# Kernel tuning notes

Measured on AMD Instinct MI355X. Metric: run time of the kernel, lower is better.

The kernel has to match this reference:

```python
import jax, jax.numpy as jnp
import numpy as np

B, S, D_MODEL = 4, 1024, 1024
HEADS, D_KEY, D_VAL = 16, 64, 64


def setup_inputs() -> dict:
    key = jax.random.key(0)
    ks = jax.random.split(key, 8)
    # glorot-ish scaled params
    sk = 1.0 / np.sqrt(D_MODEL)
    X = jax.random.normal(ks[0], (B, S, D_MODEL), dtype=jnp.float32)
    Wk = jax.random.normal(ks[1], (HEADS, D_MODEL, D_KEY), dtype=jnp.float32) * sk
    Wq = jax.random.normal(ks[2], (HEADS, D_MODEL, D_KEY), dtype=jnp.float32) * sk
    Wv = jax.random.normal(ks[3], (HEADS, D_MODEL, D_VAL), dtype=jnp.float32) * sk
    bk = jnp.zeros((HEADS, D_KEY), dtype=jnp.float32)
    bq = jnp.zeros((HEADS, D_KEY), dtype=jnp.float32)
    bv = jnp.zeros((HEADS, D_VAL), dtype=jnp.float32)
    Wo = jax.random.normal(ks[4], (HEADS * D_VAL, D_MODEL), dtype=jnp.float32) * (1.0 / np.sqrt(HEADS * D_VAL))
    bo = jnp.zeros((D_MODEL,), dtype=jnp.float32)
    return {"X": X, "Wk": Wk, "bk": bk, "Wq": Wq, "bq": bq, "Wv": Wv, "bv": bv, "Wo": Wo, "bo": bo}


def reference(X, Wk, bk, Wq, bq, Wv, bv, Wo, bo):
    # Per-head projections, batched over heads (original loops in Python)
    K = jnp.einsum('bsd,hdk->bhsk', X, Wk) + bk[None, :, None, :]
    Q = jnp.einsum('bsd,hdk->bhsk', X, Wq) + bq[None, :, None, :]
    V = jnp.einsum('bsd,hdv->bhsv', X, Wv) + bv[None, :, None, :]
    d_k = K.shape[-1]
    scores = jnp.einsum('bhqk,bhsk->bhqs', Q, K) / jnp.sqrt(jnp.asarray(d_k, X.dtype))
    A = jax.nn.softmax(scores, axis=-1)           # [B,H,S,S]
    Z = jnp.einsum('bhqs,bhsv->bhqv', A, V)        # [B,H,S,Dv]
    # concat heads: [B,S,H*Dv]
    Zc = jnp.transpose(Z, (0, 2, 1, 3)).reshape(X.shape[0], X.shape[1], -1)
    # output projection + residual; dropout is identity at inference
    return Zc @ Wo + bo + X
```

## Files before the change

### kernel.cpp

```cpp
#include <hip/hip_runtime.h>
#include <hip/hip_bf16.h>

typedef __bf16 bf16x8 __attribute__((ext_vector_type(8)));
typedef float f32x4 __attribute__((ext_vector_type(4)));
typedef unsigned short u16;
typedef u16 u16x4 __attribute__((ext_vector_type(4)));
typedef u16 u16x8 __attribute__((ext_vector_type(8)));

#define LDA 72

__device__ inline u16 f2bf(float f) {
    union { float f; unsigned u; } v; v.f = f;
    unsigned r = v.u + 0x7fffu + ((v.u >> 16) & 1u);
    return (u16)(r >> 16);
}

#define GLD16(g, l) __builtin_amdgcn_global_load_lds( \
    (const __attribute__((address_space(1))) unsigned int*)(g), \
    (__attribute__((address_space(3))) unsigned int*)(l), 16, 0, 0)

__global__ void k_prep(const float* __restrict__ X, u16* __restrict__ Xb,
                       const float* __restrict__ Wk, const float* __restrict__ Wq,
                       const float* __restrict__ Wv, u16* __restrict__ WT,
                       const float* __restrict__ Wo, u16* __restrict__ WoT) {
    __shared__ u16 Ls[64 * LDA];
    int u = blockIdx.x, tid = threadIdx.x;
    if (u < 4096) {
        int idx = u * 256 + tid;
        float4 v = *(const float4*)&X[(size_t)idx * 4];
        u16x4 o; o.x = f2bf(v.x); o.y = f2bf(v.y); o.z = f2bf(v.z); o.w = f2bf(v.w);
        *(u16x4*)&Xb[(size_t)idx * 4] = o;
    } else if (u < 4864) {
        int b2 = u - 4096;
        int dt = b2 & 15, h = (b2 >> 4) & 15, p = b2 >> 8;
        const float* src = (p == 0 ? Wk : p == 1 ? Wq : Wv);
        int r0 = tid >> 4, c4 = tid & 15;
        for (int j = 0; j < 4; j++) {
            int d = r0 + j * 16;
            float4 v = *(const float4*)&src[((size_t)h * 1024 + dt * 64 + d) * 64 + c4 * 4];
            u16* q = &Ls[d * LDA + c4 * 4];
            q[0] = f2bf(v.x); q[1] = f2bf(v.y); q[2] = f2bf(v.z); q[3] = f2bf(v.w);
        }
        __syncthreads();
        int nk = tid >> 2, cd = tid & 3;
        u16 tmp[16];
        for (int j = 0; j < 16; j++) tmp[j] = Ls[(cd * 16 + j) * LDA + nk];
        size_t o = ((size_t)(p * 1024 + h * 64 + nk)) * 1024 + dt * 64 + cd * 16;
        *(u16x8*)&WT[o] = *(u16x8*)&tmp[0];
        *(u16x8*)&WT[o + 8] = *(u16x8*)&tmp[8];
    } else {
        int b2 = u - 4864;
        int dt = b2 & 15, nt2 = b2 >> 4;
        int r0 = tid >> 4, c4 = tid & 15;
        for (int j = 0; j < 4; j++) {
            int d = r0 + j * 16;
            float4 v = *(const float4*)&Wo[(size_t)(dt * 64 + d) * 1024 + nt2 * 64 + c4 * 4];
            u16* q = &Ls[d * LDA + c4 * 4];
            q[0] = f2bf(v.x); q[1] = f2bf(v.y); q[2] = f2bf(v.z); q[3] = f2bf(v.w);
        }
        __syncthreads();
        int nr = tid >> 2, cd = tid & 3;
        u16 tmp[16];
        for (int j = 0; j < 16; j++) tmp[j] = Ls[(cd * 16 + j) * LDA + nr];
        size_t o = ((size_t)(nt2 * 64 + nr)) * 1024 + dt * 64 + cd * 16;
        *(u16x8*)&WoT[o] = *(u16x8*)&tmp[0];
        *(u16x8*)&WoT[o + 8] = *(u16x8*)&tmp[8];
    }
}

__global__ __launch_bounds__(256, 3) void k_qkv(
    const u16* __restrict__ Xb, const u16* __restrict__ WT,
    const float* __restrict__ bk, const float* __restrict__ bq, const float* __restrict__ bv,
    u16* __restrict__ Kw, u16* __restrict__ Qw, u16* __restrict__ Vtw)
{
    __shared__ u16 As[128 * 64];
    __shared__ u16 Bs[128 * 64];
    int tid = threadIdx.x, w = tid >> 6, lane = tid & 63, quad = lane >> 4, l16 = lane & 15;
    int wm = w & 1, wn = w >> 1;
    int m0 = blockIdx.x * 128, n0 = blockIdx.y * 128;
    int rl = lane >> 3, ch = lane & 7, swch = ch ^ rl;
    const u16* Ag = Xb + (size_t)(m0 + w * 32 + rl) * 1024 + swch * 8;
    const u16* Bg = WT + (size_t)(n0 + w * 32 + rl) * 1024 + swch * 8;

    int hb = blockIdx.y * 2 + wn;
    int p = hb >> 4, hh = hb & 15;
    bool ct = (p < 2);

    f32x4 acc[4][4] = {};
    for (int k0 = 0; k0 < 1024; k0 += 64) {
        for (int i = 0; i < 4; i++) {
            GLD16(Ag + (size_t)i * 8 * 1024 + k0, &As[(w * 32 + i * 8) * 64]);
            GLD16(Bg + (size_t)i * 8 * 1024 + k0, &Bs[(w * 32 + i * 8) * 64]);
        }
        __syncthreads();
        for (int ks = 0; ks < 2; ks++) {
            bf16x8 af[4], bf[4];
            int c = (ks << 2) | quad;
            for (int mt = 0; mt < 4; mt++) {
                int row = wm * 64 + mt * 16 + l16;
                af[mt] = *(bf16x8*)&As[row * 64 + (c ^ (row & 7)) * 8];
            }
            for (int nt = 0; nt < 4; nt++) {
                int row = wn * 64 + nt * 16 + l16;
                bf[nt] = *(bf16x8*)&Bs[row * 64 + (c ^ (row & 7)) * 8];
            }
            if (ct) {
                for (int mt = 0; mt < 4; mt++)
                    for (int nt = 0; nt < 4; nt++)
                        acc[mt][nt] = __builtin_amdgcn_mfma_f32_16x16x32_bf16(bf[nt], af[mt], acc[mt][nt], 0, 0, 0);
            } else {
                for (int mt = 0; mt < 4; mt++)
                    for (int nt = 0; nt < 4; nt++)
                        acc[mt][nt] = __builtin_amdgcn_mfma_f32_16x16x32_bf16(af[mt], bf[nt], acc[mt][nt], 0, 0, 0);
            }
        }
        __syncthreads();
    }
    const float* bias = (p == 0 ? bk : p == 1 ? bq : bv) + hh * 64;
    if (ct) {
        u16* dst = (p == 0) ? Kw : Qw;
        float sc = (p == 0) ? 0.125f : 1.0f;
        for (int mt = 0; mt < 4; mt++) {
            int m = m0 + wm * 64 + mt * 16 + l16;
            int b = m >> 10, s = m & 1023;
            size_t base = ((size_t)((b << 4) + hh) * 1024 + s) * 64;
            for (int nt = 0; nt < 4; nt++) {
                float4 bb = *(const float4*)&bias[nt * 16 + quad * 4];
                u16x4 o;
                o[0] = f2bf((acc[mt][nt][0] + bb.x) * sc);
                o[1] = f2bf((acc[mt][nt][1] + bb.y) * sc);
                o[2] = f2bf((acc[mt][nt][2] + bb.z) * sc);
                o[3] = f2bf((acc[mt][nt][3] + bb.w) * sc);
                *(u16x4*)&dst[base + nt * 16 + quad * 4] = o;
            }
        }
    } else {
        for (int mt = 0; mt < 4; mt++)
            for (int nt = 0; nt < 4; nt++) {
                int nk = nt * 16 + l16;
                float bb = bias[nk];
                int mb = m0 + wm * 64 + mt * 16 + quad * 4;
                int b = mb >> 10, s = mb & 1023;
                u16x4 o;
                for (int r = 0; r < 4; r++) o[r] = f2bf(acc[mt][nt][r] + bb);
                *(u16x4*)&Vtw[((size_t)((b << 4) + hh) * 64 + nk) * 1024 + s] = o;
            }
    }
}

__global__ __launch_bounds__(256) void k_attn(
    const u16* __restrict__ Qw, const u16* __restrict__ Kw,
    const u16* __restrict__ Vtw, u16* __restrict__ Zw)
{
    __shared__ u16 Ks[2][64 * 64];
    __shared__ u16 Vs[2][64 * 64];
    __shared__ u16 Ps[4 * 2 * 16 * LDA];
    int tid = threadIdx.x, w = tid >> 6, lane = tid & 63, quad = lane >> 4, l16 = lane & 15;
    int bh = blockIdx.x, q0 = blockIdx.y * 128;
    const u16* Qp = Qw + (size_t)bh * 65536;
    int rl = lane >> 3, ch = lane & 7, swch = ch ^ rl;
    const u16* Kg = Kw + (size_t)bh * 65536 + (w * 16 + rl) * 64 + swch * 8;
    const u16* Vg = Vtw + (size_t)bh * 65536 + (size_t)(w * 16 + rl) * 1024 + swch * 8;

    bf16x8 aq[2][2];
    for (int g = 0; g < 2; g++)
        for (int ks = 0; ks < 2; ks++)
            aq[g][ks] = *(const bf16x8*)&Qp[(size_t)(q0 + w * 32 + g * 16 + l16) * 64 + ks * 32 + quad * 8];

    f32x4 acc[2][4] = {};
    f32x4 accs[2] = {};
    __bf16 onev = (__bf16)1.0f;
    bf16x8 ones = {onev, onev, onev, onev, onev, onev, onev, onev};
    u16* Pw0 = Ps + (w * 2) * 16 * LDA;
    u16* Pw1 = Pw0 + 16 * LDA;

#define STAGE(st, buf) { int s0_ = (st) * 64; \
    for (int i = 0; i < 2; i++) { \
        GLD16(Kg + (s0_ + i * 8) * 64, &Ks[buf][(w * 16 + i * 8) * 64]); \
        GLD16(Vg + (size_t)i * 8 * 1024 + s0_, &Vs[buf][(w * 16 + i * 8) * 64]); } }

    STAGE(0, 0);
    for (int st = 0; st < 16; st++) {
        int buf = st & 1;
        __syncthreads();
        if (st < 15) STAGE(st + 1, buf ^ 1);
        f32x4 sacc[2][4] = {};
        for (int ks = 0; ks < 2; ks++) {
            int c = (ks << 2) | quad;
            for (int nt = 0; nt < 4; nt++) {
                int row = nt * 16 + l16;
                bf16x8 kf = *(bf16x8*)&Ks[buf][row * 64 + (c ^ (row & 7)) * 8];
                sacc[0][nt] = __builtin_amdgcn_mfma_f32_16x16x32_bf16(aq[0][ks], kf, sacc[0][nt], 0, 0, 0);
                sacc[1][nt] = __builtin_amdgcn_mfma_f32_16x16x32_bf16(aq[1][ks], kf, sacc[1][nt], 0, 0, 0);
            }
        }
        for (int g = 0; g < 2; g++) {
            u16* Pw = g ? Pw1 : Pw0;
            for (int nt = 0; nt < 4; nt++)
                for (int r = 0; r < 4; r++) {
                    float p = __builtin_exp2f(__builtin_fmaf(sacc[g][nt][r], 1.44269504f, -23.0831206f));
                    union { float f; unsigned u; } cv; cv.f = p;
                    Pw[(quad * 4 + r) * LDA + nt * 16 + l16] = (u16)((cv.u + 0x8000u) >> 16);
                }
        }
        for (int ks2 = 0; ks2 < 2; ks2++) {
            int c = (ks2 << 2) | quad;
            bf16x8 ap0 = *(bf16x8*)&Pw0[l16 * LDA + ks2 * 32 + quad * 8];
            bf16x8 ap1 = *(bf16x8*)&Pw1[l16 * LDA + ks2 * 32 + quad * 8];
            accs[0] = __builtin_amdgcn_mfma_f32_16x16x32_bf16(ap0, ones, accs[0], 0, 0, 0);
            accs[1] = __builtin_amdgcn_mfma_f32_16x16x32_bf16(ap1, ones, accs[1], 0, 0, 0);
            for (int ntv = 0; ntv < 4; ntv++) {
                int row = ntv * 16 + l16;
                bf16x8 vf = *(bf16x8*)&Vs[buf][row * 64 + (c ^ (row & 7)) * 8];
                acc[0][ntv] = __builtin_amdgcn_mfma_f32_16x16x32_bf16(ap0, vf, acc[0][ntv], 0, 0, 0);
                acc[1][ntv] = __builtin_amdgcn_mfma_f32_16x16x32_bf16(ap1, vf, acc[1][ntv], 0, 0, 0);
            }
        }
    }
#undef STAGE
    int b = bh >> 4, h = bh & 15;
    for (int g = 0; g < 2; g++)
        for (int r = 0; r < 4; r++) {
            float inv = 1.f / accs[g][r];
            int q = q0 + w * 32 + g * 16 + quad * 4 + r;
            for (int ntv = 0; ntv < 4; ntv++)
                Zw[((size_t)(b * 1024 + q)) * 1024 + h * 64 + ntv * 16 + l16] = f2bf(acc[g][ntv][r] * inv);
        }
}

__global__ __launch_bounds__(256) void k_oproj(
    const u16* __restrict__ Zw, const u16* __restrict__ WoT, const float* __restrict__ bo,
    const float* __restrict__ X, float* __restrict__ out)
{
    __shared__ u16 As[64 * 64];
    __shared__ u16 Bs[128 * 64];
    int tid = threadIdx.x, w = tid >> 6, lane = tid & 63, quad = lane >> 4, l16 = lane & 15;
    int wm = w & 1, wn = w >> 1;
    int m0 = blockIdx.x * 64, n0 = blockIdx.y * 128;
    int rl = lane >> 3, ch = lane & 7, swch = ch ^ rl;
    const u16* Ag = Zw + (size_t)(m0 + w * 16 + rl) * 1024 + swch * 8;
    const u16* Bg = WoT + (size_t)(n0 + w * 32 + rl) * 1024 + swch * 8;

    f32x4 acc[2][4] = {};
    for (int k0 = 0; k0 < 1024; k0 += 64) {
        for (int i = 0; i < 2; i++)
            GLD16(Ag + (size_t)i * 8 * 1024 + k0, &As[(w * 16 + i * 8) * 64]);
        for (int i = 0; i < 4; i++)
            GLD16(Bg + (size_t)i * 8 * 1024 + k0, &Bs[(w * 32 + i * 8) * 64]);
        __syncthreads();
        for (int ks = 0; ks < 2; ks++) {
            bf16x8 af[2], bf[4];
            int c = (ks << 2) | quad;
            for (int mt = 0; mt < 2; mt++) {
                int row = wm * 32 + mt * 16 + l16;
                af[mt] = *(bf16x8*)&As[row * 64 + (c ^ (row & 7)) * 8];
            }
            for (int nt = 0; nt < 4; nt++) {
                int row = wn * 64 + nt * 16 + l16;
                bf[nt] = *(bf16x8*)&Bs[row * 64 + (c ^ (row & 7)) * 8];
            }
            for (int mt = 0; mt < 2; mt++)
                for (int nt = 0; nt < 4; nt++)
                    acc[mt][nt] = __builtin_amdgcn_mfma_f32_16x16x32_bf16(af[mt], bf[nt], acc[mt][nt], 0, 0, 0);
        }
        __syncthreads();
    }
    for (int mt = 0; mt < 2; mt++)
        for (int nt = 0; nt < 4; nt++) {
            int n = n0 + wn * 64 + nt * 16 + l16;
            float bb = bo[n];
            for (int r = 0; r < 4; r++) {
                int m = m0 + wm * 32 + mt * 16 + quad * 4 + r;
                out[(size_t)m * 1024 + n] = acc[mt][nt][r] + bb + X[(size_t)m * 1024 + n];
            }
        }
}

extern "C" void kernel_launch(void* const* d_in, const int* in_sizes, int n_in,
                              void* d_out, int out_size, void* d_ws, size_t ws_size,
                              hipStream_t stream) {
    const float* X  = (const float*)d_in[0];
    const float* Wk = (const float*)d_in[1];
    const float* bk = (const float*)d_in[2];
    const float* Wq = (const float*)d_in[3];
    const float* bq = (const float*)d_in[4];
    const float* Wv = (const float*)d_in[5];
    const float* bv = (const float*)d_in[6];
    const float* Wo = (const float*)d_in[7];
    const float* bo = (const float*)d_in[8];
    u16* ws = (u16*)d_ws;
    const size_t NQ = 4u * 16u * 1024u * 64u;
    u16* Qw  = ws;
    u16* Kw  = ws + NQ;
    u16* Vtw = ws + 2 * NQ;
    u16* Zw  = ws + 3 * NQ;
    u16* WT  = ws + 4 * NQ;
    u16* WoT = WT + 3 * 1048576;
    u16* Xb  = WoT + 1048576;
    float* outp = (float*)d_out;

    k_prep <<<5120, 256, 0, stream>>>(X, Xb, Wk, Wq, Wv, WT, Wo, WoT);
    k_qkv  <<<dim3(32, 24), 256, 0, stream>>>(Xb, WT, bk, bq, bv, Kw, Qw, Vtw);
    k_attn <<<dim3(64, 8), 256, 0, stream>>>(Qw, Kw, Vtw, Zw);
    k_oproj<<<dim3(64, 8), 256, 0, stream>>>(Zw, WoT, bo, X, outp);
}
```

Baseline: 186.0 us.

## Load QKV A-operand fragments directly from global into registers with prefetch

The X tile in the QKV projection GEMM no longer goes through shared memory. Each wave now loads its own A fragments straight from global memory into registers and prefetches the next k-step into a second register set. This removes half the LDS traffic and shared-memory footprint, which could raise occupancy. In exchange each wave loads A redundantly, since the two wn waves share rows, it uses more VGPRs with launch bounds of 3 blocks, and it issues uncoalesced 16-byte row-strided global loads.

```diff
diff --git a/kernel.cpp b/kernel.cpp
--- a/kernel.cpp
+++ b/kernel.cpp
@@ -73,33 +73,38 @@
     const float* __restrict__ bk, const float* __restrict__ bq, const float* __restrict__ bv,
     u16* __restrict__ Kw, u16* __restrict__ Qw, u16* __restrict__ Vtw)
 {
-    __shared__ u16 As[128 * 64];
     __shared__ u16 Bs[128 * 64];
     int tid = threadIdx.x, w = tid >> 6, lane = tid & 63, quad = lane >> 4, l16 = lane & 15;
     int wm = w & 1, wn = w >> 1;
     int m0 = blockIdx.x * 128, n0 = blockIdx.y * 128;
     int rl = lane >> 3, ch = lane & 7, swch = ch ^ rl;
-    const u16* Ag = Xb + (size_t)(m0 + w * 32 + rl) * 1024 + swch * 8;
     const u16* Bg = WT + (size_t)(n0 + w * 32 + rl) * 1024 + swch * 8;
+
+    const u16* Ar[4];
+    for (int mt = 0; mt < 4; mt++)
+        Ar[mt] = Xb + (size_t)(m0 + wm * 64 + mt * 16 + l16) * 1024 + quad * 8;
 
     int hb = blockIdx.y * 2 + wn;
     int p = hb >> 4, hh = hb & 15;
     bool ct = (p < 2);
 
+    bf16x8 cur[4][2], nxt[4][2];
+    for (int mt = 0; mt < 4; mt++)
+        for (int ks = 0; ks < 2; ks++)
+            cur[mt][ks] = *(const bf16x8*)&Ar[mt][ks * 32];
+
     f32x4 acc[4][4] = {};
     for (int k0 = 0; k0 < 1024; k0 += 64) {
-        for (int i = 0; i < 4; i++) {
-            GLD16(Ag + (size_t)i * 8 * 1024 + k0, &As[(w * 32 + i * 8) * 64]);
+        for (int i = 0; i < 4; i++)
             GLD16(Bg + (size_t)i * 8 * 1024 + k0, &Bs[(w * 32 + i * 8) * 64]);
-        }
-        __syncthreads();
+        __syncthreads();
+        if (k0 < 960)
+            for (int mt = 0; mt < 4; mt++)
+                for (int ks = 0; ks < 2; ks++)
+                    nxt[mt][ks] = *(const bf16x8*)&Ar[mt][k0 + 64 + ks * 32];
         for (int ks = 0; ks < 2; ks++) {
-            bf16x8 af[4], bf[4];
+            bf16x8 bf[4];
             int c = (ks << 2) | quad;
-            for (int mt = 0; mt < 4; mt++) {
-                int row = wm * 64 + mt * 16 + l16;
-                af[mt] = *(bf16x8*)&As[row * 64 + (c ^ (row & 7)) * 8];
-            }
             for (int nt = 0; nt < 4; nt++) {
                 int row = wn * 64 + nt * 16 + l16;
                 bf[nt] = *(bf16x8*)&Bs[row * 64 + (c ^ (row & 7)) * 8];
@@ -107,14 +112,17 @@
             if (ct) {
                 for (int mt = 0; mt < 4; mt++)
                     for (int nt = 0; nt < 4; nt++)
-                        acc[mt][nt] = __builtin_amdgcn_mfma_f32_16x16x32_bf16(bf[nt], af[mt], acc[mt][nt], 0, 0, 0);
+                        acc[mt][nt] = __builtin_amdgcn_mfma_f32_16x16x32_bf16(bf[nt], cur[mt][ks], acc[mt][nt], 0, 0, 0);
             } else {
                 for (int mt = 0; mt < 4; mt++)
                     for (int nt = 0; nt < 4; nt++)
-                        acc[mt][nt] = __builtin_amdgcn_mfma_f32_16x16x32_bf16(af[mt], bf[nt], acc[mt][nt], 0, 0, 0);
-            }
-        }
-        __syncthreads();
+                        acc[mt][nt] = __builtin_amdgcn_mfma_f32_16x16x32_bf16(cur[mt][ks], bf[nt], acc[mt][nt], 0, 0, 0);
+            }
+        }
+        __syncthreads();
+        for (int mt = 0; mt < 4; mt++)
+            for (int ks = 0; ks < 2; ks++)
+                cur[mt][ks] = nxt[mt][ks];
     }
     const float* bias = (p == 0 ? bk : p == 1 ? bq : bv) + hh * 64;
     if (ct) {
```

Measured after the change: 345.6 us. +85.8%, slower.
